# Kernel optimization log

Hardware: AMD Instinct MI355X
Metric: run time of the kernel (lower is better)

Reference implementation:

```python
import jax, jax.numpy as jnp
import numpy as np

SEQ, BATCH, D_IN, D_HID, D_OUT = 2048, 256, 512, 512, 1000


def setup_inputs() -> dict:
    key = jax.random.key(0)
    ks = jax.random.split(key, 15)
    s_in = 1.0 / np.sqrt(D_IN)
    s_h = 1.0 / np.sqrt(D_HID)
    def lin(k, fan_in, shape, scale):
        return jax.random.uniform(k, shape, jnp.float32, -scale, scale)
    return {
        "x": jax.random.normal(ks[0], (SEQ, BATCH, D_IN), jnp.float32),
        # weights stored as [in, out] so y = x @ W + b
        "Wz": lin(ks[1], D_IN, (D_IN, D_HID), s_in),  "bz": lin(ks[2], D_IN, (D_HID,), s_in),
        "Uz": lin(ks[3], D_HID, (D_HID, D_HID), s_h), "buz": lin(ks[4], D_HID, (D_HID,), s_h),
        "Wr": lin(ks[5], D_IN, (D_IN, D_HID), s_in),  "br": lin(ks[6], D_IN, (D_HID,), s_in),
        "Ur": lin(ks[7], D_HID, (D_HID, D_HID), s_h), "bur": lin(ks[8], D_HID, (D_HID,), s_h),
        "Wh": lin(ks[9], D_IN, (D_IN, D_HID), s_in),  "bh": lin(ks[10], D_IN, (D_HID,), s_in),
        "Uh": lin(ks[11], D_HID, (D_HID, D_HID), s_h), "buh": lin(ks[12], D_HID, (D_HID,), s_h),
        "Wfc": lin(ks[13], D_HID, (D_HID, D_OUT), s_h), "bfc": lin(ks[14], D_HID, (D_OUT,), s_h),
    }


def reference(x, Wz, bz, Uz, buz, Wr, br, Ur, bur, Wh, bh, Uh, buh, Wfc, bfc):
    B, H = x.shape[1], Uz.shape[0]

    def gru_step(h, xt):
        # xt: [B, D_IN], h: [B, H]
        z = jax.nn.sigmoid(xt @ Wz + bz + h @ Uz + buz)
        r = jax.nn.sigmoid(xt @ Wr + br + h @ Ur + bur)
        h_tild = jnp.tanh(xt @ Wh + bh + (r * h) @ Uh + buh)
        h_new = (1.0 - z) * h + z * h_tild
        return h_new, None

    h0 = jnp.zeros((B, H), x.dtype)  # zero init hidden (broadcast-equivalent)
    h, _ = jax.lax.scan(gru_step, h0, x)
    out = jax.nn.relu(h) @ Wfc + bfc        # [B, D_OUT]
    out = out[None]                          # [1, B, D_OUT]
    return jax.nn.log_softmax(out, axis=1)  # dim=1 as in torch module
```

## Files before the change

### kernel.cpp

```cpp
#include <hip/hip_runtime.h>


typedef unsigned short ushort_t;
typedef unsigned int uint_t;
typedef __bf16 bf16_t;
typedef bf16_t bf16x8 __attribute__((ext_vector_type(8)));
typedef float f32x4 __attribute__((ext_vector_type(4)));
typedef uint_t u32x4 __attribute__((ext_vector_type(4)));

__device__ __forceinline__ ushort_t f2bf(float f) {
  uint_t u = __float_as_uint(f);
  u += 0x7FFFu + ((u >> 16) & 1u);
  return (ushort_t)(u >> 16);
}
__device__ __forceinline__ float bfu2f(uint_t h) { return __uint_as_float(h << 16); }

__device__ __forceinline__ uint_t atom_add_ret(uint_t* p, uint_t v) {
  uint_t old;
  asm volatile("global_atomic_add %0, %1, %2, off sc0\n\t"
               "s_waitcnt vmcnt(0)"
               : "=v"(old) : "v"(p), "v"(v) : "memory");
  return old;
}
__device__ __forceinline__ void atom_add_noret(uint_t* p, uint_t v) {
  asm volatile("global_atomic_add %0, %1, off" :: "v"(p), "v"(v) : "memory");
}

#define GLOAD_U16(dst, ptr, off) \
  asm volatile("global_load_ushort %0, %1, off offset:" #off : "=v"(dst) : "v"(ptr))

__global__ __launch_bounds__(256) void prep_kernel(
    const float* __restrict__ Wz, const float* __restrict__ Wr, const float* __restrict__ Wh,
    const float* __restrict__ Uz, const float* __restrict__ Ur, const float* __restrict__ Uh,
    const float* __restrict__ bz, const float* __restrict__ buz,
    const float* __restrict__ br, const float* __restrict__ bur,
    const float* __restrict__ bh, const float* __restrict__ buh,
    ushort_t* __restrict__ UT, ushort_t* __restrict__ WT, float* __restrict__ gbias)
{
  const int idx = blockIdx.x * 256 + threadIdx.x;
  {
    const int gate = idx >> 18, n = (idx >> 9) & 511, k = idx & 511;
    const float* U = (gate == 0) ? Uz : (gate == 1 ? Ur : Uh);
    UT[idx] = f2bf(U[k * 512 + n]);
  }
  {
    const int n = idx >> 9, k = idx & 511;
    const int gate = n >> 9, nn = n & 511;
    const float* W = (gate == 0) ? Wz : (gate == 1 ? Wr : Wh);
    WT[idx] = f2bf(W[k * 512 + nn]);
  }
  if (idx < 1536) {
    const int gate = idx >> 9, nn = idx & 511;
    gbias[idx] = (gate == 0) ? (bz[nn] + buz[nn])
               : (gate == 1) ? (br[nn] + bur[nn])
                             : (bh[nn] + buh[nn]);
  }
}

__global__ __launch_bounds__(256) void gate_gemm(
    const float* __restrict__ x,
    const ushort_t* __restrict__ WT,
    const float* __restrict__ gbias,
    ushort_t* __restrict__ gout,
    int mtiles)
{
  __shared__ ushort_t A_sh[128 * 72];
  __shared__ ushort_t B_sh[128 * 72];
  const int bid = blockIdx.x;
  int mt, nt;
  if ((mtiles & 31) == 0) {
    const int sb = bid / 384;
    const int r = bid - sb * 384;
    mt = sb * 32 + (r & 31);
    nt = r >> 5;
  } else {
    mt = bid / 12;
    nt = bid - mt * 12;
  }
  const int mrow0 = mt * 128;
  const int ncol0 = nt * 128;
  const int tid = threadIdx.x;
  const int wid = tid >> 6;
  const int lane = tid & 63;
  const int wm = wid >> 1, wn = wid & 1;
  const int l15 = lane & 15, l4 = lane >> 4;

  const f32x4 vzero = {0.f, 0.f, 0.f, 0.f};
  f32x4 acc[4][4];
#pragma unroll
  for (int m = 0; m < 4; ++m)
#pragma unroll
    for (int n = 0; n < 4; ++n) acc[m][n] = vzero;

  const int ar = tid >> 4, ak = tid & 15;
  const int bn = tid >> 3, bk = tid & 7;

  for (int ks = 0; ks < 8; ++ks) {
    if (ks) __syncthreads();
    const int k0 = ks * 64;
#pragma unroll
    for (int p = 0; p < 8; ++p) {
      const int r = p * 16 + ar;
      const float4 v = *(const float4*)&x[(size_t)(mrow0 + r) * 512 + (k0 + ak * 4)];
      ushort4 hv;
      hv.x = f2bf(v.x); hv.y = f2bf(v.y); hv.z = f2bf(v.z); hv.w = f2bf(v.w);
      *(ushort4*)&A_sh[r * 72 + ak * 4] = hv;
    }
#pragma unroll
    for (int p = 0; p < 4; ++p) {
      const int n = p * 32 + bn;
      *(uint4*)&B_sh[n * 72 + bk * 8] =
          *(const uint4*)&WT[(size_t)(ncol0 + n) * 512 + (k0 + bk * 8)];
    }
    __syncthreads();
#pragma unroll
    for (int kk = 0; kk < 2; ++kk) {
      bf16x8 a[4], b[4];
#pragma unroll
      for (int m = 0; m < 4; ++m)
        a[m] = *(const bf16x8*)&A_sh[(wm * 64 + m * 16 + l15) * 72 + kk * 32 + l4 * 8];
#pragma unroll
      for (int n = 0; n < 4; ++n)
        b[n] = *(const bf16x8*)&B_sh[(wn * 64 + n * 16 + l15) * 72 + kk * 32 + l4 * 8];
#pragma unroll
      for (int m = 0; m < 4; ++m)
#pragma unroll
        for (int n = 0; n < 4; ++n)
          acc[m][n] = __builtin_amdgcn_mfma_f32_16x16x32_bf16(a[m], b[n], acc[m][n], 0, 0, 0);
    }
  }
#pragma unroll
  for (int n = 0; n < 4; ++n) {
    const int gcol = ncol0 + wn * 64 + n * 16 + l15;
    const float bv = gbias[gcol];
#pragma unroll
    for (int m = 0; m < 4; ++m) {
      const int grow = mrow0 + wm * 64 + m * 16 + l4 * 4;
#pragma unroll
      for (int q = 0; q < 4; ++q)
        gout[(size_t)(grow + q) * 1536 + gcol] = f2bf(acc[m][n][q] + bv);
    }
  }
}

__device__ __forceinline__ bool group_barrier(uint_t* ctr, uint_t target, int tid, int* s_dead) {
  asm volatile("s_waitcnt vmcnt(0)" ::: "memory");
  __syncthreads();
  if (tid == 0) {
    atom_add_noret(ctr, 1u);
    int cnt = 0;
    for (;;) {
      const uint_t seen = atom_add_ret(ctr, 0u);
      if (seen >= target) break;
      __builtin_amdgcn_s_sleep(1);
      if (++cnt > (1 << 15)) { *s_dead = 1; break; }
    }
  }
  __syncthreads();
  return *s_dead != 0;
}

__device__ __forceinline__ void stage16x512(const ushort_t* __restrict__ src, int g,
                                            ushort_t* dst_lds, int tid) {
  const ushort_t* p[4];
#pragma unroll
  for (int k = 0; k < 4; ++k) {
    const int idx = tid + (k << 8);
    const int r = idx >> 6, kc = idx & 63;
    p[k] = src + (((g * 16 + r) << 9) + kc * 8);
  }
  u32x4 v0, v1, v2, v3;
  asm volatile(
      "global_load_dwordx4 %0, %4, off sc0\n\t"
      "global_load_dwordx4 %1, %5, off sc0\n\t"
      "global_load_dwordx4 %2, %6, off sc0\n\t"
      "global_load_dwordx4 %3, %7, off sc0\n\t"
      "s_waitcnt vmcnt(0)"
      : "=&v"(v0), "=&v"(v1), "=&v"(v2), "=&v"(v3)
      : "v"(p[0]), "v"(p[1]), "v"(p[2]), "v"(p[3])
      : "memory");
#pragma unroll
  for (int k = 0; k < 4; ++k) {
    const int idx = tid + (k << 8);
    const int r = idx >> 6, kc = idx & 63;
    *(u32x4*)&dst_lds[r * 520 + kc * 8] = (k == 0) ? v0 : (k == 1) ? v1 : (k == 2) ? v2 : v3;
  }
}

__global__ __launch_bounds__(256, 1) void gru_rec(
    const ushort_t* __restrict__ UT,
    const ushort_t* __restrict__ gates,
    ushort_t* __restrict__ h_buf,
    ushort_t* __restrict__ rh_buf,
    float* __restrict__ h_state,
    uint_t* __restrict__ bars,
    int Tc, int first)
{
  __shared__ ushort_t h_st[16 * 520];
  __shared__ float z_sh[512];
  __shared__ float hown[512];
  __shared__ float red[512];
  __shared__ int s_dead;

  const int tid = threadIdx.x;
  const int bid = blockIdx.x;
  const int g = bid & 15;
  const int j = bid >> 4;
  const int wid = tid >> 6;
  const int lane = tid & 63;
  const int l15 = lane & 15;
  const int l4 = lane >> 4;
  if (tid == 0) s_dead = 0;

  uint_t* ctr = bars + g * 64;
  uint_t nbar = 0;

  const int p1gate = wid >> 1;
  const int p1nt = wid & 1;
  const int p2nt = wid >> 1;
  const int p2kh = wid & 1;

  bf16x8 UB[16];
  {
    const size_t base = (size_t)((p1gate << 9) + j * 32 + p1nt * 16 + l15) * 512 + (size_t)(l4 * 8);
#pragma unroll
    for (int kk = 0; kk < 16; ++kk) UB[kk] = *(const bf16x8*)&UT[base + (size_t)kk * 32];
  }
  bf16x8 UH[8];
  {
    const size_t base = (size_t)(1024 + j * 32 + p2nt * 16 + l15) * 512 + (size_t)(p2kh * 256 + l4 * 8);
#pragma unroll
    for (int kk = 0; kk < 8; ++kk) UH[kk] = *(const bf16x8*)&UT[base + (size_t)kk * 32];
  }

  if (first) {
    for (int i = tid; i < 512; i += 256) {
      const int r = i >> 5, c = i & 31;
      h_buf[((g * 16 + r) << 9) + j * 32 + c] = 0;
      hown[i] = 0.f;
    }
  } else {
    for (int i = tid; i < 512; i += 256) {
      const int r = i >> 5, c = i & 31;
      hown[i] = h_state[((g * 16 + r) << 9) + j * 32 + c];
    }
  }
  if (group_barrier(ctr, (++nbar) * 16, tid, &s_dead)) return;

  const int colg1 = j * 32 + p1nt * 16 + l15;
  const int colg2 = j * 32 + p2nt * 16 + l15;

  uint_t c1u[4], c2u[4], n1u[4], n2u[4];
  {
    const size_t gb = (size_t)(g * 16) * 1536;
#pragma unroll
    for (int q = 0; q < 4; ++q) {
      n1u[q] = gates[gb + (size_t)(l4 * 4 + q) * 1536 + (p1gate << 9) + colg1];
      n2u[q] = gates[gb + (size_t)(l4 * 4 + q) * 1536 + 1024 + colg2];
    }
  }

  for (int tt = 0; tt < Tc; ++tt) {
    stage16x512(h_buf, g, h_st, tid);
    __syncthreads();
#pragma unroll
    for (int q = 0; q < 4; ++q) { c1u[q] = n1u[q]; c2u[q] = n2u[q]; }
    {
      const ushort_t* ap = &h_st[l15 * 520 + l4 * 8];
      f32x4 a0 = {0.f, 0.f, 0.f, 0.f}, a1 = {0.f, 0.f, 0.f, 0.f};
#pragma unroll
      for (int kk = 0; kk < 16; kk += 2) {
        a0 = __builtin_amdgcn_mfma_f32_16x16x32_bf16(*(const bf16x8*)(ap + kk * 32), UB[kk], a0, 0, 0, 0);
        a1 = __builtin_amdgcn_mfma_f32_16x16x32_bf16(*(const bf16x8*)(ap + kk * 32 + 32), UB[kk + 1], a1, 0, 0, 0);
      }
      const f32x4 acc = a0 + a1;
      const int lc = p1nt * 16 + l15;
#pragma unroll
      for (int q = 0; q < 4; ++q) {
        const int row = l4 * 4 + q;
        const float pre = acc[q] + bfu2f(c1u[q]);
        const float s = 1.f / (1.f + __expf(-pre));
        if (p1gate == 0) z_sh[row * 32 + lc] = s;
        else rh_buf[((g * 16 + row) << 9) + j * 32 + lc] = f2bf(s * hown[row * 32 + lc]);
      }
    }
    if (group_barrier(ctr, (++nbar) * 16, tid, &s_dead)) break;

    stage16x512(rh_buf, g, h_st, tid);
    __syncthreads();
    {
      const ushort_t* ap = &h_st[l15 * 520 + p2kh * 256 + l4 * 8];
      f32x4 a0 = {0.f, 0.f, 0.f, 0.f}, a1 = {0.f, 0.f, 0.f, 0.f};
#pragma unroll
      for (int kk = 0; kk < 8; kk += 2) {
        a0 = __builtin_amdgcn_mfma_f32_16x16x32_bf16(*(const bf16x8*)(ap + kk * 32), UH[kk], a0, 0, 0, 0);
        a1 = __builtin_amdgcn_mfma_f32_16x16x32_bf16(*(const bf16x8*)(ap + kk * 32 + 32), UH[kk + 1], a1, 0, 0, 0);
      }
      const f32x4 acc = a0 + a1;
      if (p2kh == 1) {
#pragma unroll
        for (int q = 0; q < 4; ++q) red[p2nt * 256 + (l4 * 4 + q) * 16 + l15] = acc[q];
      }
      __syncthreads();
      if (p2kh == 0) {
        const int lc = p2nt * 16 + l15;
#pragma unroll
        for (int q = 0; q < 4; ++q) {
          const int row = l4 * 4 + q;
          const float dot = acc[q] + red[p2nt * 256 + row * 16 + l15];
          float pre = dot + bfu2f(c2u[q]);
          pre = fminf(15.f, fmaxf(-15.f, pre));
          const float e = __expf(2.f * pre);
          const float th = (e - 1.f) / (e + 1.f);
          const float z = z_sh[row * 32 + lc];
          const float hold = hown[row * 32 + lc];
          const float hnew = (1.f - z) * hold + z * th;
          hown[row * 32 + lc] = hnew;
          h_buf[((g * 16 + row) << 9) + j * 32 + lc] = f2bf(hnew);
          if (tt == Tc - 1) h_state[((g * 16 + row) << 9) + j * 32 + lc] = hnew;
        }
      }
    }

    asm volatile("s_waitcnt vmcnt(0)" ::: "memory");
    if (tt + 1 < Tc) {
      const size_t gb = (size_t)((size_t)(tt + 1) * 256 + g * 16) * 1536;
      const ushort_t* b1  = &gates[gb + (size_t)(l4 * 4) * 1536 + (p1gate << 9) + colg1];
      const ushort_t* b1c = b1 + 2 * 1536;
      const ushort_t* b2  = &gates[gb + (size_t)(l4 * 4) * 1536 + 1024 + colg2];
      const ushort_t* b2c = b2 + 2 * 1536;
      GLOAD_U16(n1u[0], b1, 0);   GLOAD_U16(n1u[1], b1, 3072);
      GLOAD_U16(n1u[2], b1c, 0);  GLOAD_U16(n1u[3], b1c, 3072);
      GLOAD_U16(n2u[0], b2, 0);   GLOAD_U16(n2u[1], b2, 3072);
      GLOAD_U16(n2u[2], b2c, 0);  GLOAD_U16(n2u[3], b2c, 3072);
    }
    __syncthreads();
    if (tid == 0) {
      atom_add_noret(ctr, 1u);
      const uint_t target = (++nbar) * 16;
      int cnt = 0;
      for (;;) {
        const uint_t seen = atom_add_ret(ctr, 0u);
        if (seen >= target) break;
        __builtin_amdgcn_s_sleep(1);
        if (++cnt > (1 << 15)) { s_dead = 1; break; }
      }
    } else {
      ++nbar;
    }
    __syncthreads();
    if (s_dead) break;
  }
}

__global__ __launch_bounds__(256) void fc_kernel(
    const float* __restrict__ h, const float* __restrict__ Wfc,
    const float* __restrict__ bfc, float* __restrict__ logits)
{
  __shared__ float hsh[16][520];
  const int tid = threadIdx.x;
  const int by = blockIdx.y;
  {
    const int r = tid >> 4, seg = tid & 15;
    const float* src = &h[(size_t)(by * 16 + r) * 512 + seg * 32];
#pragma unroll
    for (int i = 0; i < 8; ++i) {
      float4 v = *(const float4*)&src[i * 4];
      v.x = fmaxf(v.x, 0.f); v.y = fmaxf(v.y, 0.f);
      v.z = fmaxf(v.z, 0.f); v.w = fmaxf(v.w, 0.f);
      *(float4*)&hsh[r][seg * 32 + i * 4] = v;
    }
  }
  __syncthreads();
  const int c = tid & 63, rq = tid >> 6;
  const int gc = blockIdx.x * 64 + c;
  if (gc >= 1000) return;
  float acc0 = 0.f, acc1 = 0.f, acc2 = 0.f, acc3 = 0.f;
  for (int k = 0; k < 512; ++k) {
    const float w = Wfc[(size_t)k * 1000 + gc];
    acc0 += hsh[rq * 4 + 0][k] * w;
    acc1 += hsh[rq * 4 + 1][k] * w;
    acc2 += hsh[rq * 4 + 2][k] * w;
    acc3 += hsh[rq * 4 + 3][k] * w;
  }
  const float bv = bfc[gc];
  const int r0 = by * 16 + rq * 4;
  logits[(size_t)(r0 + 0) * 1000 + gc] = acc0 + bv;
  logits[(size_t)(r0 + 1) * 1000 + gc] = acc1 + bv;
  logits[(size_t)(r0 + 2) * 1000 + gc] = acc2 + bv;
  logits[(size_t)(r0 + 3) * 1000 + gc] = acc3 + bv;
}

__global__ __launch_bounds__(256) void lsm_kernel(const float* __restrict__ logits,
                                                  float* __restrict__ out)
{
  const int c = blockIdx.x, tid = threadIdx.x;
  const int wid = tid >> 6, lane = tid & 63;
  __shared__ float red[8];
  const float v = logits[(size_t)tid * 1000 + c];
  float m = v;
#pragma unroll
  for (int o = 32; o >= 1; o >>= 1) m = fmaxf(m, __shfl_xor(m, o));
  if (lane == 0) red[wid] = m;
  __syncthreads();
  m = fmaxf(fmaxf(red[0], red[1]), fmaxf(red[2], red[3]));
  float s = __expf(v - m);
#pragma unroll
  for (int o = 32; o >= 1; o >>= 1) s += __shfl_xor(s, o);
  if (lane == 0) red[4 + wid] = s;
  __syncthreads();
  s = red[4] + red[5] + red[6] + red[7];
  out[(size_t)tid * 1000 + c] = (v - m) - __logf(s);
}

extern "C" void kernel_launch(void* const* d_in, const int* in_sizes, int n_in,
                              void* d_out, int out_size, void* d_ws, size_t ws_size,
                              hipStream_t stream) {
  (void)in_sizes; (void)n_in; (void)out_size;
  const float* x   = (const float*)d_in[0];
  const float* Wz  = (const float*)d_in[1];
  const float* bz  = (const float*)d_in[2];
  const float* Uz  = (const float*)d_in[3];
  const float* buz = (const float*)d_in[4];
  const float* Wr  = (const float*)d_in[5];
  const float* br  = (const float*)d_in[6];
  const float* Ur  = (const float*)d_in[7];
  const float* bur = (const float*)d_in[8];
  const float* Wh  = (const float*)d_in[9];
  const float* bh  = (const float*)d_in[10];
  const float* Uh  = (const float*)d_in[11];
  const float* buh = (const float*)d_in[12];
  const float* Wfc = (const float*)d_in[13];
  const float* bfc = (const float*)d_in[14];
  float* out = (float*)d_out;
  char* ws = (char*)d_ws;

  ushort_t* UT     = (ushort_t*)(ws + 0);
  ushort_t* WT     = (ushort_t*)(ws + 1572864);
  float*    gbias  = (float*)(ws + 3145728);
  ushort_t* h_buf  = (ushort_t*)(ws + 3151872);
  ushort_t* rh_buf = (ushort_t*)(ws + 3414016);
  float*    hstate = (float*)(ws + 3676160);
  float*    logits = (float*)(ws + 4200448);
  uint_t*   bars   = (uint_t*)(ws + 5224448);
  ushort_t* gates  = (ushort_t*)(ws + 5228544);

  const size_t fixed = 5228544;
  const size_t per_step = (size_t)256 * 1536 * 2;
  int Tc_max = 2048;
  if (ws_size < fixed + (size_t)2048 * per_step) {
    const size_t avail = (ws_size > fixed) ? (ws_size - fixed) : 0;
    Tc_max = (int)(avail / per_step);
    Tc_max &= ~15;
    if (Tc_max < 16) Tc_max = 16;
  }

  prep_kernel<<<3072, 256, 0, stream>>>(Wz, Wr, Wh, Uz, Ur, Uh,
                                        bz, buz, br, bur, bh, buh, UT, WT, gbias);

  int done = 0;
  while (done < 2048) {
    const int Tc = (2048 - done < Tc_max) ? (2048 - done) : Tc_max;
    const int mtiles = Tc * 2;
    gate_gemm<<<mtiles * 12, 256, 0, stream>>>(x + (size_t)done * 256 * 512, WT, gbias, gates, mtiles);
    hipMemsetAsync(bars, 0, 4096, stream);
    gru_rec<<<256, 256, 0, stream>>>(UT, gates, h_buf, rh_buf, hstate, bars, Tc, done == 0 ? 1 : 0);
    done += Tc;
  }
  fc_kernel<<<dim3(16, 16), 256, 0, stream>>>(hstate, Wfc, bfc, logits);
  lsm_kernel<<<1000, 256, 0, stream>>>(logits, out);
}
```

Before: 9.939 ms.

## Use 128 GRU blocks of 512 threads, 64 columns each, halving barrier participants

The recurrent kernel now launches 128 workgroups of 512 threads instead of 256 of 256. Each workgroup owns 64 hidden columns, using 8 waves instead of 4. The LDS staging of the 16x512 hidden tile is split across twice as many threads. Each batch-group barrier now waits on 8 workgroups instead of 16, which is meant to cut the cost of the two inter-block syncs per timestep. In exchange it uses half as many CUs and puts more waves and LDS traffic on each one.

```diff
diff --git a/kernel.cpp b/kernel.cpp
--- a/kernel.cpp
+++ b/kernel.cpp
@@ -162,32 +162,22 @@
 
 __device__ __forceinline__ void stage16x512(const ushort_t* __restrict__ src, int g,
                                             ushort_t* dst_lds, int tid) {
-  const ushort_t* p[4];
-#pragma unroll
-  for (int k = 0; k < 4; ++k) {
-    const int idx = tid + (k << 8);
-    const int r = idx >> 6, kc = idx & 63;
-    p[k] = src + (((g * 16 + r) << 9) + kc * 8);
-  }
-  u32x4 v0, v1, v2, v3;
+  const int r0 = tid >> 6, kc = tid & 63;
+  const ushort_t* p0 = src + (((g * 16 + r0) << 9) + kc * 8);
+  const ushort_t* p1 = src + (((g * 16 + r0 + 8) << 9) + kc * 8);
+  u32x4 v0, v1;
   asm volatile(
-      "global_load_dwordx4 %0, %4, off sc0\n\t"
-      "global_load_dwordx4 %1, %5, off sc0\n\t"
-      "global_load_dwordx4 %2, %6, off sc0\n\t"
-      "global_load_dwordx4 %3, %7, off sc0\n\t"
+      "global_load_dwordx4 %0, %2, off sc0\n\t"
+      "global_load_dwordx4 %1, %3, off sc0\n\t"
       "s_waitcnt vmcnt(0)"
-      : "=&v"(v0), "=&v"(v1), "=&v"(v2), "=&v"(v3)
-      : "v"(p[0]), "v"(p[1]), "v"(p[2]), "v"(p[3])
+      : "=&v"(v0), "=&v"(v1)
+      : "v"(p0), "v"(p1)
       : "memory");
-#pragma unroll
-  for (int k = 0; k < 4; ++k) {
-    const int idx = tid + (k << 8);
-    const int r = idx >> 6, kc = idx & 63;
-    *(u32x4*)&dst_lds[r * 520 + kc * 8] = (k == 0) ? v0 : (k == 1) ? v1 : (k == 2) ? v2 : v3;
-  }
-}
-
-__global__ __launch_bounds__(256, 1) void gru_rec(
+  *(u32x4*)&dst_lds[r0 * 520 + kc * 8] = v0;
+  *(u32x4*)&dst_lds[(r0 + 8) * 520 + kc * 8] = v1;
+}
+
+__global__ __launch_bounds__(512, 1) void gru_rec(
     const ushort_t* __restrict__ UT,
     const ushort_t* __restrict__ gates,
     ushort_t* __restrict__ h_buf,
@@ -197,9 +187,9 @@
     int Tc, int first)
 {
   __shared__ ushort_t h_st[16 * 520];
-  __shared__ float z_sh[512];
-  __shared__ float hown[512];
-  __shared__ float red[512];
+  __shared__ float z_sh[1024];
+  __shared__ float hown[1024];
+  __shared__ float red[1024];
   __shared__ int s_dead;
 
   const int tid = threadIdx.x;
@@ -215,48 +205,48 @@
   uint_t* ctr = bars + g * 64;
   uint_t nbar = 0;
 
-  const int p1gate = wid >> 1;
-  const int p1nt = wid & 1;
+  const int p1gate = wid >> 2;
+  const int p1nt = wid & 3;
   const int p2nt = wid >> 1;
   const int p2kh = wid & 1;
 
   bf16x8 UB[16];
   {
-    const size_t base = (size_t)((p1gate << 9) + j * 32 + p1nt * 16 + l15) * 512 + (size_t)(l4 * 8);
+    const size_t base = (size_t)((p1gate << 9) + j * 64 + p1nt * 16 + l15) * 512 + (size_t)(l4 * 8);
 #pragma unroll
     for (int kk = 0; kk < 16; ++kk) UB[kk] = *(const bf16x8*)&UT[base + (size_t)kk * 32];
   }
   bf16x8 UH[8];
   {
-    const size_t base = (size_t)(1024 + j * 32 + p2nt * 16 + l15) * 512 + (size_t)(p2kh * 256 + l4 * 8);
+    const size_t base = (size_t)(1024 + j * 64 + p2nt * 16 + l15) * 512 + (size_t)(p2kh * 256 + l4 * 8);
 #pragma unroll
     for (int kk = 0; kk < 8; ++kk) UH[kk] = *(const bf16x8*)&UT[base + (size_t)kk * 32];
   }
 
   if (first) {
-    for (int i = tid; i < 512; i += 256) {
-      const int r = i >> 5, c = i & 31;
-      h_buf[((g * 16 + r) << 9) + j * 32 + c] = 0;
+    for (int i = tid; i < 1024; i += 512) {
+      const int r = i >> 6, c = i & 63;
+      h_buf[((g * 16 + r) << 9) + j * 64 + c] = 0;
       hown[i] = 0.f;
     }
   } else {
-    for (int i = tid; i < 512; i += 256) {
-      const int r = i >> 5, c = i & 31;
-      hown[i] = h_state[((g * 16 + r) << 9) + j * 32 + c];
-    }
-  }
-  if (group_barrier(ctr, (++nbar) * 16, tid, &s_dead)) return;
-
-  const int colg1 = j * 32 + p1nt * 16 + l15;
-  const int colg2 = j * 32 + p2nt * 16 + l15;
+    for (int i = tid; i < 1024; i += 512) {
+      const int r = i >> 6, c = i & 63;
+      hown[i] = h_state[((g * 16 + r) << 9) + j * 64 + c];
+    }
+  }
+  if (group_barrier(ctr, (++nbar) * 8, tid, &s_dead)) return;
+
+  const int colg1 = (p1gate << 9) + j * 64 + p1nt * 16 + l15;
+  const int colg2 = 1024 + j * 64 + p2nt * 16 + l15;
 
   uint_t c1u[4], c2u[4], n1u[4], n2u[4];
   {
     const size_t gb = (size_t)(g * 16) * 1536;
 #pragma unroll
     for (int q = 0; q < 4; ++q) {
-      n1u[q] = gates[gb + (size_t)(l4 * 4 + q) * 1536 + (p1gate << 9) + colg1];
-      n2u[q] = gates[gb + (size_t)(l4 * 4 + q) * 1536 + 1024 + colg2];
+      n1u[q] = gates[gb + (size_t)(l4 * 4 + q) * 1536 + colg1];
+      n2u[q] = gates[gb + (size_t)(l4 * 4 + q) * 1536 + colg2];
     }
   }
 
@@ -280,11 +270,11 @@
         const int row = l4 * 4 + q;
         const float pre = acc[q] + bfu2f(c1u[q]);
         const float s = 1.f / (1.f + __expf(-pre));
-        if (p1gate == 0) z_sh[row * 32 + lc] = s;
-        else rh_buf[((g * 16 + row) << 9) + j * 32 + lc] = f2bf(s * hown[row * 32 + lc]);
-      }
-    }
-    if (group_barrier(ctr, (++nbar) * 16, tid, &s_dead)) break;
+        if (p1gate == 0) z_sh[row * 64 + lc] = s;
+        else rh_buf[((g * 16 + row) << 9) + j * 64 + lc] = f2bf(s * hown[row * 64 + lc]);
+      }
+    }
+    if (group_barrier(ctr, (++nbar) * 8, tid, &s_dead)) break;
 
     stage16x512(rh_buf, g, h_st, tid);
     __syncthreads();
@@ -312,12 +302,12 @@
           pre = fminf(15.f, fmaxf(-15.f, pre));
           const float e = __expf(2.f * pre);
           const float th = (e - 1.f) / (e + 1.f);
-          const float z = z_sh[row * 32 + lc];
-          const float hold = hown[row * 32 + lc];
+          const float z = z_sh[row * 64 + lc];
+          const float hold = hown[row * 64 + lc];
           const float hnew = (1.f - z) * hold + z * th;
-          hown[row * 32 + lc] = hnew;
-          h_buf[((g * 16 + row) << 9) + j * 32 + lc] = f2bf(hnew);
-          if (tt == Tc - 1) h_state[((g * 16 + row) << 9) + j * 32 + lc] = hnew;
+          hown[row * 64 + lc] = hnew;
+          h_buf[((g * 16 + row) << 9) + j * 64 + lc] = f2bf(hnew);
+          if (tt == Tc - 1) h_state[((g * 16 + row) << 9) + j * 64 + lc] = hnew;
         }
       }
     }
@@ -325,9 +315,9 @@
     asm volatile("s_waitcnt vmcnt(0)" ::: "memory");
     if (tt + 1 < Tc) {
       const size_t gb = (size_t)((size_t)(tt + 1) * 256 + g * 16) * 1536;
-      const ushort_t* b1  = &gates[gb + (size_t)(l4 * 4) * 1536 + (p1gate << 9) + colg1];
+      const ushort_t* b1  = &gates[gb + (size_t)(l4 * 4) * 1536 + colg1];
       const ushort_t* b1c = b1 + 2 * 1536;
-      const ushort_t* b2  = &gates[gb + (size_t)(l4 * 4) * 1536 + 1024 + colg2];
+      const ushort_t* b2  = &gates[gb + (size_t)(l4 * 4) * 1536 + colg2];
       const ushort_t* b2c = b2 + 2 * 1536;
       GLOAD_U16(n1u[0], b1, 0);   GLOAD_U16(n1u[1], b1, 3072);
       GLOAD_U16(n1u[2], b1c, 0);  GLOAD_U16(n1u[3], b1c, 3072);
@@ -337,7 +327,7 @@
     __syncthreads();
     if (tid == 0) {
       atom_add_noret(ctr, 1u);
-      const uint_t target = (++nbar) * 16;
+      const uint_t target = (++nbar) * 8;
       int cnt = 0;
       for (;;) {
         const uint_t seen = atom_add_ret(ctr, 0u);
@@ -464,7 +454,7 @@
     const int mtiles = Tc * 2;
     gate_gemm<<<mtiles * 12, 256, 0, stream>>>(x + (size_t)done * 256 * 512, WT, gbias, gates, mtiles);
     hipMemsetAsync(bars, 0, 4096, stream);
-    gru_rec<<<256, 256, 0, stream>>>(UT, gates, h_buf, rh_buf, hstate, bars, Tc, done == 0 ? 1 : 0);
+    gru_rec<<<128, 512, 0, stream>>>(UT, gates, h_buf, rh_buf, hstate, bars, Tc, done == 0 ? 1 : 0);
     done += Tc;
   }
   fc_kernel<<<dim3(16, 16), 256, 0, stream>>>(hstate, Wfc, bfc, logits);
```

New measurement: 10.45 ms. 1.05x slower.

## Replace shared-counter group barrier with per-block flag barrier polled by a wavefront

Applied to the files above, without the earlier changes.

The single shared atomic counter per group, which every block incremented and thread 0 polled with sleeps, is replaced by one counter per block. Each block bumps only its own counter, and the first wavefront polls all 16 peer counters in parallel lanes without sleeping. This is meant to cut atomic contention and wake-up latency on the three grid barriers in every timestep. The prefetch of the next step's gate values moves earlier, before the Uh MFMA phase, using plain loads instead of inline asm, so its latency overlaps compute. The flag array grows, so the workspace offsets and the memset size are enlarged to match.

```diff
diff --git a/kernel.cpp b/kernel.cpp
--- a/kernel.cpp
+++ b/kernel.cpp
@@ -25,9 +25,6 @@
 __device__ __forceinline__ void atom_add_noret(uint_t* p, uint_t v) {
   asm volatile("global_atomic_add %0, %1, off" :: "v"(p), "v"(v) : "memory");
 }
-
-#define GLOAD_U16(dst, ptr, off) \
-  asm volatile("global_load_ushort %0, %1, off offset:" #off : "=v"(dst) : "v"(ptr))
 
 __global__ __launch_bounds__(256) void prep_kernel(
     const float* __restrict__ Wz, const float* __restrict__ Wr, const float* __restrict__ Wh,
@@ -143,16 +140,17 @@
   }
 }
 
-__device__ __forceinline__ bool group_barrier(uint_t* ctr, uint_t target, int tid, int* s_dead) {
+__device__ __forceinline__ bool flag_barrier(uint_t* gflags, int j, int lane, int wid, int tid,
+                                             uint_t nbar, int* s_dead) {
   asm volatile("s_waitcnt vmcnt(0)" ::: "memory");
   __syncthreads();
-  if (tid == 0) {
-    atom_add_noret(ctr, 1u);
+  if (tid == 0) atom_add_noret(gflags + j * 16, 1u);
+  if (wid == 0) {
     int cnt = 0;
     for (;;) {
-      const uint_t seen = atom_add_ret(ctr, 0u);
-      if (seen >= target) break;
-      __builtin_amdgcn_s_sleep(1);
+      uint_t v = nbar;
+      if (lane < 16) v = atom_add_ret(gflags + lane * 16, 0u);
+      if (!__any(v < nbar)) break;
       if (++cnt > (1 << 15)) { *s_dead = 1; break; }
     }
   }
@@ -212,7 +210,7 @@
   const int l4 = lane >> 4;
   if (tid == 0) s_dead = 0;
 
-  uint_t* ctr = bars + g * 64;
+  uint_t* gflags = bars + g * 256;
   uint_t nbar = 0;
 
   const int p1gate = wid >> 1;
@@ -245,7 +243,8 @@
       hown[i] = h_state[((g * 16 + r) << 9) + j * 32 + c];
     }
   }
-  if (group_barrier(ctr, (++nbar) * 16, tid, &s_dead)) return;
+  ++nbar;
+  if (flag_barrier(gflags, j, lane, wid, tid, nbar, &s_dead)) return;
 
   const int colg1 = j * 32 + p1nt * 16 + l15;
   const int colg2 = j * 32 + p2nt * 16 + l15;
@@ -284,10 +283,19 @@
         else rh_buf[((g * 16 + row) << 9) + j * 32 + lc] = f2bf(s * hown[row * 32 + lc]);
       }
     }
-    if (group_barrier(ctr, (++nbar) * 16, tid, &s_dead)) break;
+    ++nbar;
+    if (flag_barrier(gflags, j, lane, wid, tid, nbar, &s_dead)) break;
 
     stage16x512(rh_buf, g, h_st, tid);
     __syncthreads();
+    if (tt + 1 < Tc) {
+      const size_t gb = (size_t)((size_t)(tt + 1) * 256 + g * 16) * 1536;
+#pragma unroll
+      for (int q = 0; q < 4; ++q) {
+        n1u[q] = gates[gb + (size_t)(l4 * 4 + q) * 1536 + (p1gate << 9) + colg1];
+        n2u[q] = gates[gb + (size_t)(l4 * 4 + q) * 1536 + 1024 + colg2];
+      }
+    }
     {
       const ushort_t* ap = &h_st[l15 * 520 + p2kh * 256 + l4 * 8];
       f32x4 a0 = {0.f, 0.f, 0.f, 0.f}, a1 = {0.f, 0.f, 0.f, 0.f};
@@ -321,35 +329,8 @@
         }
       }
     }
-
-    asm volatile("s_waitcnt vmcnt(0)" ::: "memory");
-    if (tt + 1 < Tc) {
-      const size_t gb = (size_t)((size_t)(tt + 1) * 256 + g * 16) * 1536;
-      const ushort_t* b1  = &gates[gb + (size_t)(l4 * 4) * 1536 + (p1gate << 9) + colg1];
-      const ushort_t* b1c = b1 + 2 * 1536;
-      const ushort_t* b2  = &gates[gb + (size_t)(l4 * 4) * 1536 + 1024 + colg2];
-      const ushort_t* b2c = b2 + 2 * 1536;
-      GLOAD_U16(n1u[0], b1, 0);   GLOAD_U16(n1u[1], b1, 3072);
-      GLOAD_U16(n1u[2], b1c, 0);  GLOAD_U16(n1u[3], b1c, 3072);
-      GLOAD_U16(n2u[0], b2, 0);   GLOAD_U16(n2u[1], b2, 3072);
-      GLOAD_U16(n2u[2], b2c, 0);  GLOAD_U16(n2u[3], b2c, 3072);
-    }
-    __syncthreads();
-    if (tid == 0) {
-      atom_add_noret(ctr, 1u);
-      const uint_t target = (++nbar) * 16;
-      int cnt = 0;
-      for (;;) {
-        const uint_t seen = atom_add_ret(ctr, 0u);
-        if (seen >= target) break;
-        __builtin_amdgcn_s_sleep(1);
-        if (++cnt > (1 << 15)) { s_dead = 1; break; }
-      }
-    } else {
-      ++nbar;
-    }
-    __syncthreads();
-    if (s_dead) break;
+    ++nbar;
+    if (flag_barrier(gflags, j, lane, wid, tid, nbar, &s_dead)) break;
   }
 }
 
@@ -443,9 +424,9 @@
   float*    hstate = (float*)(ws + 3676160);
   float*    logits = (float*)(ws + 4200448);
   uint_t*   bars   = (uint_t*)(ws + 5224448);
-  ushort_t* gates  = (ushort_t*)(ws + 5228544);
-
-  const size_t fixed = 5228544;
+  ushort_t* gates  = (ushort_t*)(ws + 5240832);
+
+  const size_t fixed = 5240832;
   const size_t per_step = (size_t)256 * 1536 * 2;
   int Tc_max = 2048;
   if (ws_size < fixed + (size_t)2048 * per_step) {
@@ -463,7 +444,7 @@
     const int Tc = (2048 - done < Tc_max) ? (2048 - done) : Tc_max;
     const int mtiles = Tc * 2;
     gate_gemm<<<mtiles * 12, 256, 0, stream>>>(x + (size_t)done * 256 * 512, WT, gbias, gates, mtiles);
-    hipMemsetAsync(bars, 0, 4096, stream);
+    hipMemsetAsync(bars, 0, 16384, stream);
     gru_rec<<<256, 256, 0, stream>>>(UT, gates, h_buf, rh_buf, hstate, bars, Tc, done == 0 ? 1 : 0);
     done += Tc;
   }
```

Result: slower. 10.90 ms (+9.6%).
